# Optimization experiments

Measured on AMD Instinct MI355X. Metric: run time of the kernel, lower is better.

Reference implementation:

```python
import jax, jax.numpy as jnp
import numpy as np

T, B, D_IN, H = 1024, 64, 256, 256
D_CAT = D_IN + H  # input to each gate MLP


def setup_inputs() -> dict:
    key = jax.random.key(0)
    k_x, k_w1, k_w2 = jax.random.split(key, 3)
    inputs = jax.random.normal(k_x, (T, B, D_IN), dtype=jnp.float32)
    # 4 gates (forget, input, update, output), weights stacked on leading axis.
    # Layout: W1[g] is (in, out) so combined @ W1[g] + b1[g].
    W1 = jax.random.normal(k_w1, (4, D_CAT, H), dtype=jnp.float32) * (1.0 / np.sqrt(D_CAT))
    b1 = jnp.zeros((4, H), dtype=jnp.float32)
    W2 = jax.random.normal(k_w2, (4, H, H), dtype=jnp.float32) * (1.0 / np.sqrt(H))
    b2 = jnp.zeros((4, H), dtype=jnp.float32)
    return {"inputs": inputs, "W1": W1, "b1": b1, "W2": W2, "b2": b2}


def reference(inputs, W1, b1, W2, b2):
    """HybridQLSTM forward. inputs: [T, B, D_IN]. Returns (stacked [T,B,H], (hx, cx))."""
    Bsz = inputs.shape[1]
    h0 = jnp.zeros((Bsz, H), dtype=inputs.dtype)
    c0 = jnp.zeros((Bsz, H), dtype=inputs.dtype)

    def step(carry, x):
        hx, cx = carry
        combined = jnp.concatenate([x, hx], axis=1)  # [B, D_CAT]
        # All 4 gate MLPs at once: sigmoid(W2 @ tanh(W1 @ combined + b1) + b2)
        hid = jnp.tanh(jnp.einsum('bd,gdh->gbh', combined, W1) + b1[:, None, :])
        gates = jax.nn.sigmoid(jnp.einsum('gbh,ghk->gbk', hid, W2) + b2[:, None, :])
        f, i, u, o = gates[0], gates[1], gates[2], gates[3]
        g = jnp.tanh(u)  # faithful: tanh applied on top of sampler sigmoid
        cx = f * cx + i * g
        hx = o * jnp.tanh(cx)
        return (hx, cx), hx

    (hx, cx), stacked = jax.lax.scan(step, (h0, c0), inputs)
    return stacked, (hx, cx)
```

## Files before the change

### kernel.cpp

```cpp
#include <hip/hip_runtime.h>
#include <math.h>


#define TS   1024
#define BB   64
#define HH   256
#define NELEM (BB*HH)

typedef __attribute__((ext_vector_type(8))) short bf16x8;
typedef __attribute__((ext_vector_type(4))) float f32x4;
typedef unsigned long long u64;
typedef unsigned int u32;
typedef unsigned short u16;

__device__ __forceinline__ u64 ld_a8(const u64* p) {
    return __hip_atomic_load(p, __ATOMIC_RELAXED, __HIP_MEMORY_SCOPE_AGENT);
}
__device__ __forceinline__ u32 ld_a4(const u32* p) {
    return __hip_atomic_load(p, __ATOMIC_RELAXED, __HIP_MEMORY_SCOPE_AGENT);
}
__device__ __forceinline__ void st_a4(u32* p, u32 v) {
    __hip_atomic_store(p, v, __ATOMIC_RELAXED, __HIP_MEMORY_SCOPE_AGENT);
}
__device__ __forceinline__ void st_a2(u16* p, u16 v) {
    __hip_atomic_store(p, v, __ATOMIC_RELAXED, __HIP_MEMORY_SCOPE_AGENT);
}

__device__ __forceinline__ void gbar(int e, int bid, int tid, int* arr) {
    __syncthreads();
    if (tid == 0)
        __hip_atomic_store(&arr[bid * 16], e, __ATOMIC_RELAXED, __HIP_MEMORY_SCOPE_AGENT);
    if (tid < 64) {
        int v;
        do {
            v = __hip_atomic_load(&arr[tid * 16], __ATOMIC_RELAXED, __HIP_MEMORY_SCOPE_AGENT);
        } while (!__all(v >= e));
    }
    __syncthreads();
    asm volatile("" ::: "memory");
}

__device__ __forceinline__ void cvt8(const float* a, bf16x8& hi, bf16x8& lo) {
#pragma unroll
    for (int i = 0; i < 8; ++i) {
        unsigned u = __builtin_bit_cast(unsigned, a[i]);
        unsigned short h = (unsigned short)(u >> 16);
        float hf = __builtin_bit_cast(float, (unsigned)h << 16);
        float lf = a[i] - hf;
        unsigned short l2 = (unsigned short)(__builtin_bit_cast(unsigned, lf) >> 16);
        hi[i] = (short)h;
        lo[i] = (short)l2;
    }
}
__device__ __forceinline__ f32x4 mf3(bf16x8 ah, bf16x8 al, bf16x8 bh, bf16x8 bl, f32x4 acc) {
    acc = __builtin_amdgcn_mfma_f32_16x16x32_bf16(ah, bh, acc, 0, 0, 0);
    acc = __builtin_amdgcn_mfma_f32_16x16x32_bf16(ah, bl, acc, 0, 0, 0);
    acc = __builtin_amdgcn_mfma_f32_16x16x32_bf16(al, bh, acc, 0, 0, 0);
    return acc;
}
__device__ __forceinline__ f32x4 mf2(bf16x8 ah, bf16x8 bh, bf16x8 bl, f32x4 acc) {
    acc = __builtin_amdgcn_mfma_f32_16x16x32_bf16(ah, bh, acc, 0, 0, 0);
    acc = __builtin_amdgcn_mfma_f32_16x16x32_bf16(ah, bl, acc, 0, 0, 0);
    return acc;
}

__global__ __launch_bounds__(256) void qinit(u32* hpack, int* flags) {
    int i = blockIdx.x * 256 + threadIdx.x;
    st_a4(&hpack[i], 0u);
    if (i < 64 * 16)
        __hip_atomic_store(&flags[i], 0, __ATOMIC_RELAXED, __HIP_MEMORY_SCOPE_AGENT);
}

__global__ __launch_bounds__(256, 1) void qlstm_persist(
    const float* __restrict__ x,
    const float* __restrict__ W1,
    const float* __restrict__ b1,
    const float* __restrict__ W2,
    const float* __restrict__ b2,
    float* __restrict__ out,
    u32* __restrict__ hpack,
    u16* __restrict__ hid_hi,
    u32* __restrict__ gatesq,
    int* __restrict__ arr)
{
    const int tid = threadIdx.x;
    const int bid = blockIdx.x;
    const int g  = bid >> 4;
    const int ct = bid & 15;

    __shared__ unsigned short smem[24576];
    {
        const float* W1g = W1 + (size_t)g * 512 * 256;
        const float* W2g = W2 + (size_t)g * 256 * 256;
        for (int w = tid; w < 24 * 64; w += 256) {
            int ktu  = w >> 6;
            int lane = w & 63;
            int quad = lane >> 4, n = lane & 15;
            int col = ct * 16 + n;
            const float* src;
            int k0, base;
            if (ktu < 16) { src = W1g; k0 = ktu * 32 + quad * 8;        base = (ktu * 2) * 512; }
            else          { src = W2g; k0 = (ktu - 16) * 32 + quad * 8; base = 16384 + ((ktu - 16) * 2) * 512; }
#pragma unroll
            for (int j = 0; j < 8; ++j) {
                float f = src[(size_t)(k0 + j) * 256 + col];
                unsigned u = __builtin_bit_cast(unsigned, f);
                unsigned short h16 = (unsigned short)(u >> 16);
                float hf = __builtin_bit_cast(float, (unsigned)h16 << 16);
                float lf = f - hf;
                unsigned short l16 = (unsigned short)(__builtin_bit_cast(unsigned, lf) >> 16);
                smem[base + lane * 8 + j]       = h16;
                smem[base + 512 + lane * 8 + j] = l16;
            }
        }
        __syncthreads();
    }

    const int l    = tid & 63;
    const int wave = tid >> 6;
    const int quad = l >> 4;
    const int n15  = l & 15;
    const int brow = wave * 16 + n15;
    const int col  = ct * 16 + n15;
    const int bo   = wave * 16 + quad * 4;
    const float b1v = b1[g * 256 + col];
    const float b2v = b2[g * 256 + col];
    const int e_own = bid * 256 + tid;
    float creg = 0.0f;

    f32x4 accE = {0.f, 0.f, 0.f, 0.f};
    f32x4 accO = {0.f, 0.f, 0.f, 0.f};

    {
        const float* xr = x + (size_t)brow * 256;
#pragma unroll
        for (int kt = 0; kt < 8; ++kt) {
            float a[8];
            *(float4*)&a[0] = *(const float4*)(xr + kt * 32 + quad * 8);
            *(float4*)&a[4] = *(const float4*)(xr + kt * 32 + quad * 8 + 4);
            bf16x8 ah, al;
            cvt8(a, ah, al);
            bf16x8 bh = *(const bf16x8*)&smem[(kt * 2) * 512 + l * 8];
            bf16x8 bl = *(const bf16x8*)&smem[(kt * 2) * 512 + 512 + l * 8];
            if (kt & 1) accO = mf3(ah, al, bh, bl, accO);
            else        accE = mf3(ah, al, bh, bl, accE);
        }
    }

    for (int t = 0; t < TS; ++t) {
        gbar(3 * t, bid, tid, arr);

        {
            const u64* hp = (const u64*)(hpack + brow * 256);
#pragma unroll
            for (int kt = 8; kt < 16; ++kt) {
                int k0 = (kt - 8) * 32 + quad * 8;
                bf16x8 ah, al;
#pragma unroll
                for (int q = 0; q < 4; ++q) {
                    u64 v = ld_a8(hp + (k0 >> 1) + q);
                    u32 w0 = (u32)v, w1 = (u32)(v >> 32);
                    ah[q * 2]     = (short)(w0 & 0xffff);
                    al[q * 2]     = (short)(w0 >> 16);
                    ah[q * 2 + 1] = (short)(w1 & 0xffff);
                    al[q * 2 + 1] = (short)(w1 >> 16);
                }
                bf16x8 bh = *(const bf16x8*)&smem[(kt * 2) * 512 + l * 8];
                bf16x8 bl = *(const bf16x8*)&smem[(kt * 2) * 512 + 512 + l * 8];
                if (kt & 1) accO = mf3(ah, al, bh, bl, accO);
                else        accE = mf3(ah, al, bh, bl, accE);
            }
        }
#pragma unroll
        for (int r = 0; r < 4; ++r) {
            float v = tanhf(accE[r] + accO[r] + b1v);
            u32 u = __builtin_bit_cast(u32, v);
            st_a2(&hid_hi[(size_t)(g * 64 + bo + r) * 256 + col], (u16)((u + 0x8000u) >> 16));
        }

        gbar(3 * t + 1, bid, tid, arr);

        {
            f32x4 s2E = {0.f, 0.f, 0.f, 0.f};
            f32x4 s2O = {0.f, 0.f, 0.f, 0.f};
            const u64* hr = (const u64*)(hid_hi + (size_t)(g * 64 + brow) * 256);
#pragma unroll
            for (int kt = 0; kt < 8; ++kt) {
                int k0 = kt * 32 + quad * 8;
                bf16x8 ah;
                u64 v0 = ld_a8(hr + (k0 >> 2));
                u64 v1 = ld_a8(hr + (k0 >> 2) + 1);
#pragma unroll
                for (int q = 0; q < 4; ++q) ah[q]     = (short)((v0 >> (16 * q)) & 0xffff);
#pragma unroll
                for (int q = 0; q < 4; ++q) ah[4 + q] = (short)((v1 >> (16 * q)) & 0xffff);
                bf16x8 bh = *(const bf16x8*)&smem[16384 + (kt * 2) * 512 + l * 8];
                bf16x8 bl = *(const bf16x8*)&smem[16384 + (kt * 2) * 512 + 512 + l * 8];
                if (kt & 1) s2O = mf2(ah, bh, bl, s2O);
                else        s2E = mf2(ah, bh, bl, s2E);
            }
#pragma unroll
            for (int r = 0; r < 4; ++r) {
                float v = 1.0f / (1.0f + expf(-(s2E[r] + s2O[r] + b2v)));
                st_a4(&gatesq[(size_t)(g * 64 + bo + r) * 256 + col], __builtin_bit_cast(u32, v));
            }
        }

        gbar(3 * t + 2, bid, tid, arr);

        {
            float f = __builtin_bit_cast(float, ld_a4(gatesq + e_own));
            float i = __builtin_bit_cast(float, ld_a4(gatesq + 16384 + e_own));
            float u = __builtin_bit_cast(float, ld_a4(gatesq + 32768 + e_own));
            float o = __builtin_bit_cast(float, ld_a4(gatesq + 49152 + e_own));
            creg = f * creg + i * tanhf(u);
            float hn = o * tanhf(creg);
            u32 hu = __builtin_bit_cast(u32, hn);
            u16 h16 = (u16)(hu >> 16);
            float hf = __builtin_bit_cast(float, (u32)h16 << 16);
            float lf = hn - hf;
            u16 l16 = (u16)(__builtin_bit_cast(u32, lf) >> 16);
            st_a4(&hpack[e_own], (u32)h16 | ((u32)l16 << 16));
            out[(size_t)t * NELEM + e_own] = hn;
            if (t == TS - 1) {
                out[(size_t)TS * NELEM + e_own]         = hn;
                out[(size_t)TS * NELEM + NELEM + e_own] = creg;
            }
        }

        if (t < TS - 1) {
            accE = (f32x4){0.f, 0.f, 0.f, 0.f};
            accO = (f32x4){0.f, 0.f, 0.f, 0.f};
            const float* xr = x + ((size_t)(t + 1) * BB + brow) * 256;
#pragma unroll
            for (int kt = 0; kt < 8; ++kt) {
                float a[8];
                *(float4*)&a[0] = *(const float4*)(xr + kt * 32 + quad * 8);
                *(float4*)&a[4] = *(const float4*)(xr + kt * 32 + quad * 8 + 4);
                bf16x8 ah, al;
                cvt8(a, ah, al);
                bf16x8 bh = *(const bf16x8*)&smem[(kt * 2) * 512 + l * 8];
                bf16x8 bl = *(const bf16x8*)&smem[(kt * 2) * 512 + 512 + l * 8];
                if (kt & 1) accO = mf3(ah, al, bh, bl, accO);
                else        accE = mf3(ah, al, bh, bl, accE);
            }
        }
    }
}

extern "C" void kernel_launch(void* const* d_in, const int* in_sizes, int n_in,
                              void* d_out, int out_size, void* d_ws, size_t ws_size,
                              hipStream_t stream)
{
    const float* x  = (const float*)d_in[0];
    const float* W1 = (const float*)d_in[1];
    const float* b1 = (const float*)d_in[2];
    const float* W2 = (const float*)d_in[3];
    const float* b2 = (const float*)d_in[4];
    float* out = (float*)d_out;

    char* ws = (char*)d_ws;
    u32* hpack  = (u32*)ws;
    u16* hid_hi = (u16*)(ws + 65536);
    u32* gatesq = (u32*)(ws + 65536 + 131072);
    int* arr    = (int*)(ws + 65536 + 131072 + 262144);

    qinit<<<64, 256, 0, stream>>>(hpack, arr);
    qlstm_persist<<<64, 256, 0, stream>>>(x, W1, b1, W2, b2, out,
                                          hpack, hid_hi, gatesq, arr);
}
```

Measured before the change: 14.61 ms.

## Switch persistent QLSTM kernel to fp16 MFMA on 16 blocks with 16-bit gate exchange

Replaces the split-bf16 (hi/lo, 2–3 MFMAs per product) scheme with single fp16 MFMAs and cuts the grid from 64 to 16 blocks, each computing 64 output columns with four accumulators. Hidden state, hidden activations and quantized gates are exchanged as 16-bit values, and the cell update is vectorized four elements per thread. The grid barrier polls only 16 flags with s_sleep, drops its trailing syncthreads, and is moved to the end of the step. These changes aim to cut MFMA count, barrier participants and exchange traffic, at the cost of lower precision (fp16 weights and inputs, 16-bit fixed-point gates) and a possible accuracy or overflow risk.

```diff
diff --git a/kernel.cpp b/kernel.cpp
--- a/kernel.cpp
+++ b/kernel.cpp
@@ -2,72 +2,58 @@
 #include <math.h>
 
 
-#define TS   1024
-#define BB   64
-#define HH   256
-#define NELEM (BB*HH)
-
-typedef __attribute__((ext_vector_type(8))) short bf16x8;
-typedef __attribute__((ext_vector_type(4))) float f32x4;
+#define TS    1024
+#define NELEM 16384
+
 typedef unsigned long long u64;
 typedef unsigned int u32;
 typedef unsigned short u16;
+typedef _Float16 f16;
+typedef __attribute__((ext_vector_type(8))) _Float16 half8;
+typedef __attribute__((ext_vector_type(8))) unsigned short ushort8;
+typedef __attribute__((ext_vector_type(4))) float f32x4;
 
 __device__ __forceinline__ u64 ld_a8(const u64* p) {
     return __hip_atomic_load(p, __ATOMIC_RELAXED, __HIP_MEMORY_SCOPE_AGENT);
 }
-__device__ __forceinline__ u32 ld_a4(const u32* p) {
-    return __hip_atomic_load(p, __ATOMIC_RELAXED, __HIP_MEMORY_SCOPE_AGENT);
-}
-__device__ __forceinline__ void st_a4(u32* p, u32 v) {
+__device__ __forceinline__ void st_a8(u64* p, u64 v) {
     __hip_atomic_store(p, v, __ATOMIC_RELAXED, __HIP_MEMORY_SCOPE_AGENT);
 }
 __device__ __forceinline__ void st_a2(u16* p, u16 v) {
     __hip_atomic_store(p, v, __ATOMIC_RELAXED, __HIP_MEMORY_SCOPE_AGENT);
 }
 
-__device__ __forceinline__ void gbar(int e, int bid, int tid, int* arr) {
+__device__ __forceinline__ void gbar(int e, int bid, int tid, int* flags) {
     __syncthreads();
     if (tid == 0)
-        __hip_atomic_store(&arr[bid * 16], e, __ATOMIC_RELAXED, __HIP_MEMORY_SCOPE_AGENT);
-    if (tid < 64) {
-        int v;
-        do {
-            v = __hip_atomic_load(&arr[tid * 16], __ATOMIC_RELAXED, __HIP_MEMORY_SCOPE_AGENT);
-        } while (!__all(v >= e));
-    }
-    __syncthreads();
+        __hip_atomic_store(&flags[bid * 16], e, __ATOMIC_RELAXED, __HIP_MEMORY_SCOPE_AGENT);
+    const int l = tid & 63;
+    for (;;) {
+        int ok = 1;
+        if (l < 16) {
+            int v = __hip_atomic_load(&flags[l * 16], __ATOMIC_RELAXED, __HIP_MEMORY_SCOPE_AGENT);
+            ok = (v >= e);
+        }
+        if (__all(ok)) break;
+        __builtin_amdgcn_s_sleep(1);
+    }
     asm volatile("" ::: "memory");
 }
 
-__device__ __forceinline__ void cvt8(const float* a, bf16x8& hi, bf16x8& lo) {
-#pragma unroll
-    for (int i = 0; i < 8; ++i) {
-        unsigned u = __builtin_bit_cast(unsigned, a[i]);
-        unsigned short h = (unsigned short)(u >> 16);
-        float hf = __builtin_bit_cast(float, (unsigned)h << 16);
-        float lf = a[i] - hf;
-        unsigned short l2 = (unsigned short)(__builtin_bit_cast(unsigned, lf) >> 16);
-        hi[i] = (short)h;
-        lo[i] = (short)l2;
-    }
-}
-__device__ __forceinline__ f32x4 mf3(bf16x8 ah, bf16x8 al, bf16x8 bh, bf16x8 bl, f32x4 acc) {
-    acc = __builtin_amdgcn_mfma_f32_16x16x32_bf16(ah, bh, acc, 0, 0, 0);
-    acc = __builtin_amdgcn_mfma_f32_16x16x32_bf16(ah, bl, acc, 0, 0, 0);
-    acc = __builtin_amdgcn_mfma_f32_16x16x32_bf16(al, bh, acc, 0, 0, 0);
-    return acc;
-}
-__device__ __forceinline__ f32x4 mf2(bf16x8 ah, bf16x8 bh, bf16x8 bl, f32x4 acc) {
-    acc = __builtin_amdgcn_mfma_f32_16x16x32_bf16(ah, bh, acc, 0, 0, 0);
-    acc = __builtin_amdgcn_mfma_f32_16x16x32_bf16(ah, bl, acc, 0, 0, 0);
-    return acc;
-}
-
-__global__ __launch_bounds__(256) void qinit(u32* hpack, int* flags) {
+__device__ __forceinline__ half8 h8_from(u64 v0, u64 v1) {
+    ushort8 t;
+#pragma unroll
+    for (int q = 0; q < 4; ++q) {
+        t[q]     = (u16)(v0 >> (16 * q));
+        t[4 + q] = (u16)(v1 >> (16 * q));
+    }
+    return __builtin_bit_cast(half8, t);
+}
+
+__global__ __launch_bounds__(256) void qinit(u64* hglob, int* flags) {
     int i = blockIdx.x * 256 + threadIdx.x;
-    st_a4(&hpack[i], 0u);
-    if (i < 64 * 16)
+    st_a8(&hglob[i], 0ull);
+    if (i < 16 * 16)
         __hip_atomic_store(&flags[i], 0, __ATOMIC_RELAXED, __HIP_MEMORY_SCOPE_AGENT);
 }
 
@@ -78,58 +64,60 @@
     const float* __restrict__ W2,
     const float* __restrict__ b2,
     float* __restrict__ out,
-    u32* __restrict__ hpack,
-    u16* __restrict__ hid_hi,
-    u32* __restrict__ gatesq,
-    int* __restrict__ arr)
+    u64* __restrict__ hglob,
+    u16* __restrict__ hidg,
+    u16* __restrict__ gateq,
+    int* __restrict__ flags)
 {
     const int tid = threadIdx.x;
     const int bid = blockIdx.x;
-    const int g  = bid >> 4;
-    const int ct = bid & 15;
-
-    __shared__ unsigned short smem[24576];
+    const int g  = bid >> 2;
+    const int ct = bid & 3;
+
+    __shared__ f16 w1s[16 * 4 * 512];
+    __shared__ f16 w2s[8 * 4 * 512];
     {
         const float* W1g = W1 + (size_t)g * 512 * 256;
+        for (int i = tid; i < 16 * 4 * 64; i += 256) {
+            int kt = i >> 8, nt = (i >> 6) & 3, lane = i & 63;
+            int k0 = kt * 32 + (lane >> 4) * 8;
+            int col = ct * 64 + nt * 16 + (lane & 15);
+#pragma unroll
+            for (int j = 0; j < 8; ++j)
+                w1s[((kt * 4 + nt) * 64 + lane) * 8 + j] = (f16)W1g[(size_t)(k0 + j) * 256 + col];
+        }
         const float* W2g = W2 + (size_t)g * 256 * 256;
-        for (int w = tid; w < 24 * 64; w += 256) {
-            int ktu  = w >> 6;
-            int lane = w & 63;
-            int quad = lane >> 4, n = lane & 15;
-            int col = ct * 16 + n;
-            const float* src;
-            int k0, base;
-            if (ktu < 16) { src = W1g; k0 = ktu * 32 + quad * 8;        base = (ktu * 2) * 512; }
-            else          { src = W2g; k0 = (ktu - 16) * 32 + quad * 8; base = 16384 + ((ktu - 16) * 2) * 512; }
-#pragma unroll
-            for (int j = 0; j < 8; ++j) {
-                float f = src[(size_t)(k0 + j) * 256 + col];
-                unsigned u = __builtin_bit_cast(unsigned, f);
-                unsigned short h16 = (unsigned short)(u >> 16);
-                float hf = __builtin_bit_cast(float, (unsigned)h16 << 16);
-                float lf = f - hf;
-                unsigned short l16 = (unsigned short)(__builtin_bit_cast(unsigned, lf) >> 16);
-                smem[base + lane * 8 + j]       = h16;
-                smem[base + 512 + lane * 8 + j] = l16;
-            }
+        for (int i = tid; i < 8 * 4 * 64; i += 256) {
+            int kt = i >> 8, nt = (i >> 6) & 3, lane = i & 63;
+            int k0 = kt * 32 + (lane >> 4) * 8;
+            int col = ct * 64 + nt * 16 + (lane & 15);
+#pragma unroll
+            for (int j = 0; j < 8; ++j)
+                w2s[((kt * 4 + nt) * 64 + lane) * 8 + j] = (f16)W2g[(size_t)(k0 + j) * 256 + col];
         }
         __syncthreads();
     }
 
     const int l    = tid & 63;
-    const int wave = tid >> 6;
+    const int w    = tid >> 6;
     const int quad = l >> 4;
     const int n15  = l & 15;
-    const int brow = wave * 16 + n15;
-    const int col  = ct * 16 + n15;
-    const int bo   = wave * 16 + quad * 4;
-    const float b1v = b1[g * 256 + col];
-    const float b2v = b2[g * 256 + col];
-    const int e_own = bid * 256 + tid;
-    float creg = 0.0f;
-
-    f32x4 accE = {0.f, 0.f, 0.f, 0.f};
-    f32x4 accO = {0.f, 0.f, 0.f, 0.f};
+    const int brow = w * 16 + n15;
+    const int bo   = w * 16 + quad * 4;
+    float b1v[4], b2v[4];
+#pragma unroll
+    for (int nt = 0; nt < 4; ++nt) {
+        b1v[nt] = b1[g * 256 + ct * 64 + nt * 16 + n15];
+        b2v[nt] = b2[g * 256 + ct * 64 + nt * 16 + n15];
+    }
+    const int e0   = bid * 1024 + tid * 4;
+    const int urow = e0 >> 8;
+    const int ucol = e0 & 255;
+    float creg[4] = {0.f, 0.f, 0.f, 0.f};
+
+    f32x4 acc[4];
+#pragma unroll
+    for (int nt = 0; nt < 4; ++nt) acc[nt] = (f32x4){0.f, 0.f, 0.f, 0.f};
 
     {
         const float* xr = x + (size_t)brow * 256;
@@ -138,113 +126,120 @@
             float a[8];
             *(float4*)&a[0] = *(const float4*)(xr + kt * 32 + quad * 8);
             *(float4*)&a[4] = *(const float4*)(xr + kt * 32 + quad * 8 + 4);
-            bf16x8 ah, al;
-            cvt8(a, ah, al);
-            bf16x8 bh = *(const bf16x8*)&smem[(kt * 2) * 512 + l * 8];
-            bf16x8 bl = *(const bf16x8*)&smem[(kt * 2) * 512 + 512 + l * 8];
-            if (kt & 1) accO = mf3(ah, al, bh, bl, accO);
-            else        accE = mf3(ah, al, bh, bl, accE);
+            half8 ah;
+#pragma unroll
+            for (int j = 0; j < 8; ++j) ah[j] = (f16)a[j];
+#pragma unroll
+            for (int nt = 0; nt < 4; ++nt)
+                acc[nt] = __builtin_amdgcn_mfma_f32_16x16x32_f16(
+                    ah, *(const half8*)&w1s[((kt * 4 + nt) * 64 + l) * 8], acc[nt], 0, 0, 0);
         }
     }
 
     for (int t = 0; t < TS; ++t) {
-        gbar(3 * t, bid, tid, arr);
-
         {
-            const u64* hp = (const u64*)(hpack + brow * 256);
+            const u64* hp = hglob + brow * 64;
 #pragma unroll
             for (int kt = 8; kt < 16; ++kt) {
-                int k0 = (kt - 8) * 32 + quad * 8;
-                bf16x8 ah, al;
-#pragma unroll
-                for (int q = 0; q < 4; ++q) {
-                    u64 v = ld_a8(hp + (k0 >> 1) + q);
-                    u32 w0 = (u32)v, w1 = (u32)(v >> 32);
-                    ah[q * 2]     = (short)(w0 & 0xffff);
-                    al[q * 2]     = (short)(w0 >> 16);
-                    ah[q * 2 + 1] = (short)(w1 & 0xffff);
-                    al[q * 2 + 1] = (short)(w1 >> 16);
+                int ko = (kt - 8) * 8 + quad * 2;
+                u64 v0 = ld_a8(hp + ko);
+                u64 v1 = ld_a8(hp + ko + 1);
+                half8 ah = h8_from(v0, v1);
+#pragma unroll
+                for (int nt = 0; nt < 4; ++nt)
+                    acc[nt] = __builtin_amdgcn_mfma_f32_16x16x32_f16(
+                        ah, *(const half8*)&w1s[((kt * 4 + nt) * 64 + l) * 8], acc[nt], 0, 0, 0);
+            }
+        }
+#pragma unroll
+        for (int nt = 0; nt < 4; ++nt)
+#pragma unroll
+            for (int r = 0; r < 4; ++r) {
+                f16 v = (f16)tanhf(acc[nt][r] + b1v[nt]);
+                st_a2(&hidg[(size_t)(g * 64 + bo + r) * 256 + ct * 64 + nt * 16 + n15],
+                      __builtin_bit_cast(u16, v));
+            }
+
+        gbar(3 * t + 1, bid, tid, flags);
+
+        {
+            f32x4 s2[4];
+#pragma unroll
+            for (int nt = 0; nt < 4; ++nt) s2[nt] = (f32x4){0.f, 0.f, 0.f, 0.f};
+            const u64* hr = (const u64*)(hidg + (size_t)(g * 64 + brow) * 256);
+#pragma unroll
+            for (int kt = 0; kt < 8; ++kt) {
+                int ko = kt * 8 + quad * 2;
+                u64 v0 = ld_a8(hr + ko);
+                u64 v1 = ld_a8(hr + ko + 1);
+                half8 ah = h8_from(v0, v1);
+#pragma unroll
+                for (int nt = 0; nt < 4; ++nt)
+                    s2[nt] = __builtin_amdgcn_mfma_f32_16x16x32_f16(
+                        ah, *(const half8*)&w2s[((kt * 4 + nt) * 64 + l) * 8], s2[nt], 0, 0, 0);
+            }
+#pragma unroll
+            for (int nt = 0; nt < 4; ++nt)
+#pragma unroll
+                for (int r = 0; r < 4; ++r) {
+                    float sg = 1.0f / (1.0f + expf(-(s2[nt][r] + b2v[nt])));
+                    st_a2(&gateq[(size_t)(g * 64 + bo + r) * 256 + ct * 64 + nt * 16 + n15],
+                          (u16)(sg * 65535.0f + 0.5f));
                 }
-                bf16x8 bh = *(const bf16x8*)&smem[(kt * 2) * 512 + l * 8];
-                bf16x8 bl = *(const bf16x8*)&smem[(kt * 2) * 512 + 512 + l * 8];
-                if (kt & 1) accO = mf3(ah, al, bh, bl, accO);
-                else        accE = mf3(ah, al, bh, bl, accE);
-            }
-        }
-#pragma unroll
-        for (int r = 0; r < 4; ++r) {
-            float v = tanhf(accE[r] + accO[r] + b1v);
-            u32 u = __builtin_bit_cast(u32, v);
-            st_a2(&hid_hi[(size_t)(g * 64 + bo + r) * 256 + col], (u16)((u + 0x8000u) >> 16));
-        }
-
-        gbar(3 * t + 1, bid, tid, arr);
+        }
+
+        gbar(3 * t + 2, bid, tid, flags);
 
         {
-            f32x4 s2E = {0.f, 0.f, 0.f, 0.f};
-            f32x4 s2O = {0.f, 0.f, 0.f, 0.f};
-            const u64* hr = (const u64*)(hid_hi + (size_t)(g * 64 + brow) * 256);
-#pragma unroll
-            for (int kt = 0; kt < 8; ++kt) {
-                int k0 = kt * 32 + quad * 8;
-                bf16x8 ah;
-                u64 v0 = ld_a8(hr + (k0 >> 2));
-                u64 v1 = ld_a8(hr + (k0 >> 2) + 1);
-#pragma unroll
-                for (int q = 0; q < 4; ++q) ah[q]     = (short)((v0 >> (16 * q)) & 0xffff);
-#pragma unroll
-                for (int q = 0; q < 4; ++q) ah[4 + q] = (short)((v1 >> (16 * q)) & 0xffff);
-                bf16x8 bh = *(const bf16x8*)&smem[16384 + (kt * 2) * 512 + l * 8];
-                bf16x8 bl = *(const bf16x8*)&smem[16384 + (kt * 2) * 512 + 512 + l * 8];
-                if (kt & 1) s2O = mf2(ah, bh, bl, s2O);
-                else        s2E = mf2(ah, bh, bl, s2E);
-            }
-#pragma unroll
-            for (int r = 0; r < 4; ++r) {
-                float v = 1.0f / (1.0f + expf(-(s2E[r] + s2O[r] + b2v)));
-                st_a4(&gatesq[(size_t)(g * 64 + bo + r) * 256 + col], __builtin_bit_cast(u32, v));
-            }
-        }
-
-        gbar(3 * t + 2, bid, tid, arr);
-
-        {
-            float f = __builtin_bit_cast(float, ld_a4(gatesq + e_own));
-            float i = __builtin_bit_cast(float, ld_a4(gatesq + 16384 + e_own));
-            float u = __builtin_bit_cast(float, ld_a4(gatesq + 32768 + e_own));
-            float o = __builtin_bit_cast(float, ld_a4(gatesq + 49152 + e_own));
-            creg = f * creg + i * tanhf(u);
-            float hn = o * tanhf(creg);
-            u32 hu = __builtin_bit_cast(u32, hn);
-            u16 h16 = (u16)(hu >> 16);
-            float hf = __builtin_bit_cast(float, (u32)h16 << 16);
-            float lf = hn - hf;
-            u16 l16 = (u16)(__builtin_bit_cast(u32, lf) >> 16);
-            st_a4(&hpack[e_own], (u32)h16 | ((u32)l16 << 16));
-            out[(size_t)t * NELEM + e_own] = hn;
+            const u16* gq = gateq + urow * 256 + ucol;
+            u64 qf = ld_a8((const u64*)(gq));
+            u64 qi = ld_a8((const u64*)(gq + 16384));
+            u64 qu = ld_a8((const u64*)(gq + 32768));
+            u64 qo = ld_a8((const u64*)(gq + 49152));
+            float4 ov;
+            u64 hpack = 0;
+            const float s = 1.0f / 65535.0f;
+#pragma unroll
+            for (int k = 0; k < 4; ++k) {
+                float f = (float)((qf >> (16 * k)) & 0xffff) * s;
+                float i = (float)((qi >> (16 * k)) & 0xffff) * s;
+                float u = (float)((qu >> (16 * k)) & 0xffff) * s;
+                float o = (float)((qo >> (16 * k)) & 0xffff) * s;
+                creg[k] = f * creg[k] + i * tanhf(u);
+                float hn = o * tanhf(creg[k]);
+                ((float*)&ov)[k] = hn;
+                u16 hb = __builtin_bit_cast(u16, (f16)hn);
+                hpack |= (u64)hb << (16 * k);
+            }
+            *(float4*)(out + (size_t)t * NELEM + e0) = ov;
+            st_a8(&hglob[e0 >> 2], hpack);
             if (t == TS - 1) {
-                out[(size_t)TS * NELEM + e_own]         = hn;
-                out[(size_t)TS * NELEM + NELEM + e_own] = creg;
-            }
-        }
-
+                *(float4*)(out + (size_t)TS * NELEM + e0) = ov;
+                float4 cv = {creg[0], creg[1], creg[2], creg[3]};
+                *(float4*)(out + (size_t)TS * NELEM + NELEM + e0) = cv;
+            }
+        }
+
+#pragma unroll
+        for (int nt = 0; nt < 4; ++nt) acc[nt] = (f32x4){0.f, 0.f, 0.f, 0.f};
         if (t < TS - 1) {
-            accE = (f32x4){0.f, 0.f, 0.f, 0.f};
-            accO = (f32x4){0.f, 0.f, 0.f, 0.f};
-            const float* xr = x + ((size_t)(t + 1) * BB + brow) * 256;
+            const float* xr = x + ((size_t)(t + 1) * 64 + brow) * 256;
 #pragma unroll
             for (int kt = 0; kt < 8; ++kt) {
                 float a[8];
                 *(float4*)&a[0] = *(const float4*)(xr + kt * 32 + quad * 8);
                 *(float4*)&a[4] = *(const float4*)(xr + kt * 32 + quad * 8 + 4);
-                bf16x8 ah, al;
-                cvt8(a, ah, al);
-                bf16x8 bh = *(const bf16x8*)&smem[(kt * 2) * 512 + l * 8];
-                bf16x8 bl = *(const bf16x8*)&smem[(kt * 2) * 512 + 512 + l * 8];
-                if (kt & 1) accO = mf3(ah, al, bh, bl, accO);
-                else        accE = mf3(ah, al, bh, bl, accE);
-            }
-        }
+                half8 ah;
+#pragma unroll
+                for (int j = 0; j < 8; ++j) ah[j] = (f16)a[j];
+#pragma unroll
+                for (int nt = 0; nt < 4; ++nt)
+                    acc[nt] = __builtin_amdgcn_mfma_f32_16x16x32_f16(
+                        ah, *(const half8*)&w1s[((kt * 4 + nt) * 64 + l) * 8], acc[nt], 0, 0, 0);
+            }
+        }
+
+        gbar(3 * t + 3, bid, tid, flags);
     }
 }
 
@@ -260,12 +255,12 @@
     float* out = (float*)d_out;
 
     char* ws = (char*)d_ws;
-    u32* hpack  = (u32*)ws;
-    u16* hid_hi = (u16*)(ws + 65536);
-    u32* gatesq = (u32*)(ws + 65536 + 131072);
-    int* arr    = (int*)(ws + 65536 + 131072 + 262144);
-
-    qinit<<<64, 256, 0, stream>>>(hpack, arr);
-    qlstm_persist<<<64, 256, 0, stream>>>(x, W1, b1, W2, b2, out,
-                                          hpack, hid_hi, gatesq, arr);
-}
+    u64* hglob = (u64*)ws;
+    u16* hidg  = (u16*)(ws + 32768);
+    u16* gateq = (u16*)(ws + 32768 + 131072);
+    int* flags = (int*)(ws + 32768 + 131072 + 131072);
+
+    qinit<<<16, 256, 0, stream>>>(hglob, flags);
+    qlstm_persist<<<16, 256, 0, stream>>>(x, W1, b1, W2, b2, out,
+                                          hglob, hidg, gateq, flags);
+}
```

Result: faster. 13.57 ms (-7.2%).
